# Optimization experiments

Measured on AMD Instinct MI355X. Metric: run time of the kernel, lower is better.

Reference implementation:

```python
import jax, jax.numpy as jnp
import numpy as np

D = 3            # sheaf stalk dimension
HIDDEN = 32      # hidden_channels
OUT_SHAPE = (3, 3)
N_ROWS = 300000  # N * d rows in x
E = 3000000      # edge_index entries (multiple of D)


def setup_inputs() -> dict:
    key = jax.random.key(0)
    k1, k2, k3 = jax.random.split(key, 3)
    x = jax.random.normal(k1, (N_ROWS, HIDDEN), dtype=jnp.float32)
    edge_index = jax.random.randint(k2, (2, E), 0, N_ROWS, dtype=jnp.int64)
    # linear1: nn.Linear(2*hidden, prod(out_shape), bias=False) -> weight [9, 64]
    W = jax.random.normal(k3, (int(np.prod(OUT_SHAPE)), 2 * HIDDEN), dtype=jnp.float32) * 0.1
    return {"x": x, "edge_index": edge_index, "W": W}


def reference(x, edge_index, W):
    src, dst = edge_index[0], edge_index[1]
    x_src = x[src]                       # [E, hidden] gather
    x_dst = x[dst]                       # [E, hidden] gather
    x_cat = jnp.concatenate([x_src, x_dst], axis=-1)         # [E, 2*hidden]
    x_cat = x_cat.reshape(-1, D, 2 * HIDDEN).sum(axis=1)      # [E/d, 2*hidden]
    maps = jnp.tanh(x_cat @ W.T)                              # [E/d, 9]
    return maps.reshape(-1, OUT_SHAPE[0], OUT_SHAPE[1])       # [E/d, 3, 3]
```

## Files before the change

kernel.cpp:

```cpp
#include <hip/hip_runtime.h>
#include <hip/hip_fp16.h>

#define HIDDEN 32
#define NOUT 9

__device__ __forceinline__ float fast_tanh(float v) {
    float e = __expf(2.0f * v);
    return 1.0f - __fdividef(2.0f, e + 1.0f);
}
__device__ __forceinline__ unsigned pack2f(float a, float b) {
    unsigned lo = __half_as_ushort(__float2half(a));
    unsigned hi = __half_as_ushort(__float2half(b));
    return lo | (hi << 16);
}
__device__ __forceinline__ float2 up2(unsigned u) {
    union { unsigned u; __half2 h; } cv; cv.u = u;
    return __half22float2(cv.h);
}

__device__ __forceinline__ unsigned q14(float y) {
    float t = fminf(fmaxf(y, -7.99f), 7.99f);
    return (unsigned)(__float2int_rn(t * 1024.f) + 8192);
}
__device__ __forceinline__ uint4 pack9(const float* y) {
    unsigned f0 = q14(y[0]), f1 = q14(y[1]), f2 = q14(y[2]);
    unsigned f3 = q14(y[3]), f4 = q14(y[4]), f5 = q14(y[5]);
    unsigned f6 = q14(y[6]), f7 = q14(y[7]), f8 = q14(y[8]);
    uint4 r;
    r.x = f0 | (f1 << 14) | (f2 << 28);
    r.y = (f2 >> 4) | (f3 << 10) | (f4 << 24);
    r.z = (f4 >> 8) | (f5 << 6) | (f6 << 20);
    r.w = (f6 >> 12) | (f7 << 2) | (f8 << 16);
    return r;
}
__device__ __forceinline__ unsigned ext14(const uint4& v, int j) {
    const int bit = 14 * j;
    if (bit + 14 <= 64) {
        unsigned long long u = ((unsigned long long)v.y << 32) | v.x;
        return (unsigned)(u >> bit) & 0x3FFFu;
    } else if (bit < 64) {
        unsigned long long u = ((unsigned long long)v.z << 32) | v.y;
        return (unsigned)(u >> (bit - 32)) & 0x3FFFu;
    } else {
        unsigned long long u = ((unsigned long long)v.w << 32) | v.z;
        return (unsigned)(u >> (bit - 64)) & 0x3FFFu;
    }
}

__global__ __launch_bounds__(256) void precompute_kernel(
    const float* __restrict__ x, const float* __restrict__ W,
    uint4* __restrict__ ys16, uint4* __restrict__ yd16, int NR)
{
    __shared__ float XL[256 * 33];
    __shared__ float Wl[NOUT * 64];
    for (int i = threadIdx.x; i < NOUT * 64; i += 256) Wl[i] = W[i];

    const int base = blockIdx.x * 256;
    const float4* Xv = reinterpret_cast<const float4*>(x);
    #pragma unroll
    for (int i = 0; i < 8; ++i) {
        int f = i * 256 + threadIdx.x;
        int row = f >> 3, ch = f & 7;
        float4 v = make_float4(0.f, 0.f, 0.f, 0.f);
        if (base + row < NR) v = Xv[(size_t)(base + row) * 8 + ch];
        float* p = &XL[row * 33 + ch * 4];
        p[0] = v.x; p[1] = v.y; p[2] = v.z; p[3] = v.w;
    }
    __syncthreads();

    const int row = base + threadIdx.x;
    if (row >= NR) return;

    float ys[NOUT], yd[NOUT];
    #pragma unroll
    for (int j = 0; j < NOUT; ++j) { ys[j] = 0.f; yd[j] = 0.f; }
    const float* xr = &XL[threadIdx.x * 33];
    #pragma unroll
    for (int c = 0; c < 32; ++c) {
        float xv = xr[c];
        #pragma unroll
        for (int j = 0; j < NOUT; ++j) {
            ys[j] += xv * Wl[j * 64 + c];
            yd[j] += xv * Wl[j * 64 + 32 + c];
        }
    }
    ys16[row] = pack9(ys);
    yd16[row] = pack9(yd);
}

__global__ __launch_bounds__(256) void passA_kernel(
    const uint4* __restrict__ ys16, const int* __restrict__ ei,
    unsigned* __restrict__ pw,
    unsigned short* __restrict__ ph,
    int G)
{
    int g = blockIdx.x * 256 + threadIdx.x;
    if (g >= G) return;
    const int* sp = ei + 3 * (size_t)g;
    int s0 = __builtin_nontemporal_load(sp);
    int s1 = __builtin_nontemporal_load(sp + 1);
    int s2 = __builtin_nontemporal_load(sp + 2);

    uint4 A0 = ys16[s0], A1 = ys16[s1], A2 = ys16[s2];

    float c[NOUT];
    #pragma unroll
    for (int j = 0; j < NOUT; ++j) {
        unsigned e = ext14(A0, j) + ext14(A1, j) + ext14(A2, j);
        c[j] = (float)(int)e * (1.f / 1024.f) - 24.f;
    }

    __builtin_nontemporal_store(pack2f(c[0], c[1]), pw + g);
    __builtin_nontemporal_store(pack2f(c[2], c[3]), pw + (size_t)G + g);
    __builtin_nontemporal_store(pack2f(c[4], c[5]), pw + 2 * (size_t)G + g);
    __builtin_nontemporal_store(pack2f(c[6], c[7]), pw + 3 * (size_t)G + g);
    __builtin_nontemporal_store(__half_as_ushort(__float2half(c[8])), ph + g);
}

__global__ __launch_bounds__(256) void passB_kernel(
    const uint4* __restrict__ yd16, const int* __restrict__ ei,
    const unsigned* __restrict__ pw, const unsigned short* __restrict__ ph,
    float* __restrict__ out, int G, int E)
{
    __shared__ float OL[256 * 9];
    const int t = threadIdx.x;
    const int g = blockIdx.x * 256 + t;

    if (g < G) {
        const int* dp = ei + (size_t)E + 3 * (size_t)g;
        int d0 = __builtin_nontemporal_load(dp);
        int d1 = __builtin_nontemporal_load(dp + 1);
        int d2 = __builtin_nontemporal_load(dp + 2);

        uint4 B0 = yd16[d0], B1 = yd16[d1], B2 = yd16[d2];

        unsigned pq0 = __builtin_nontemporal_load(pw + g);
        unsigned pq1 = __builtin_nontemporal_load(pw + (size_t)G + g);
        unsigned pq2 = __builtin_nontemporal_load(pw + 2 * (size_t)G + g);
        unsigned pq3 = __builtin_nontemporal_load(pw + 3 * (size_t)G + g);
        unsigned short pq4 = __builtin_nontemporal_load(ph + g);

        float c[NOUT];
        float2 tt;
        tt = up2(pq0); c[0] = tt.x; c[1] = tt.y;
        tt = up2(pq1); c[2] = tt.x; c[3] = tt.y;
        tt = up2(pq2); c[4] = tt.x; c[5] = tt.y;
        tt = up2(pq3); c[6] = tt.x; c[7] = tt.y;
        c[8] = __half2float(__ushort_as_half(pq4));

        #pragma unroll
        for (int j = 0; j < NOUT; ++j) {
            unsigned e = ext14(B0, j) + ext14(B1, j) + ext14(B2, j);
            c[j] += (float)(int)e * (1.f / 1024.f) - 24.f;
        }

        float* o = &OL[t * 9];
        #pragma unroll
        for (int j = 0; j < NOUT; ++j) o[j] = fast_tanh(c[j]);
    } else {
        float* o = &OL[t * 9];
        #pragma unroll
        for (int j = 0; j < NOUT; ++j) o[j] = 0.f;
    }
    __syncthreads();

    const size_t base = (size_t)blockIdx.x * 256 * 9;
    const size_t lim  = (size_t)G * 9;
    #pragma unroll
    for (int k = 0; k < 9; ++k) {
        size_t d = base + (size_t)k * 256 + t;
        if (d < lim)
            __builtin_nontemporal_store(OL[k * 256 + t], out + d);
    }
}

__global__ __launch_bounds__(256) void gather1_kernel(
    const uint4* __restrict__ ys16, const uint4* __restrict__ yd16,
    const int* __restrict__ ei, float* __restrict__ out, int G, int E)
{
    int g = blockIdx.x * 256 + threadIdx.x;
    if (g >= G) return;
    const int* sp = ei + 3 * (size_t)g;
    const int* dp = ei + (size_t)E + 3 * (size_t)g;
    int s0 = sp[0], s1 = sp[1], s2 = sp[2];
    int d0 = dp[0], d1 = dp[1], d2 = dp[2];
    uint4 A0 = ys16[s0], A1 = ys16[s1], A2 = ys16[s2];
    uint4 B0 = yd16[d0], B1 = yd16[d1], B2 = yd16[d2];
    float* o = out + (size_t)g * 9;
    #pragma unroll
    for (int j = 0; j < NOUT; ++j) {
        unsigned e = ext14(A0, j) + ext14(A1, j) + ext14(A2, j)
                   + ext14(B0, j) + ext14(B1, j) + ext14(B2, j);
        o[j] = fast_tanh((float)(int)e * (1.f / 1024.f) - 48.f);
    }
}

__device__ __forceinline__ float dot4(float4 a, float4 b) {
    return a.x * b.x + a.y * b.y + a.z * b.z + a.w * b.w;
}
__global__ __launch_bounds__(256) void sheaf_fallback(
    const float* __restrict__ x, const int* __restrict__ edge_index,
    const float* __restrict__ W, float* __restrict__ out, int G, int E)
{
    __shared__ float Wlds[NOUT * 64];
    for (int i = threadIdx.x; i < NOUT * 64; i += 256) Wlds[i] = W[i];
    __syncthreads();
    const int l = threadIdx.x & 7;
    const int s = (blockIdx.x * 256 + threadIdx.x) >> 3;
    const int g0 = 2 * s, g1 = 2 * s + 1;
    if (g0 >= G) return;
    const bool has1 = (g1 < G);
    const float4* Xv = reinterpret_cast<const float4*>(x);
    const float4* Wv = reinterpret_cast<const float4*>(Wlds);
    const int* sp = edge_index + 3 * g0;
    const int* dp = edge_index + E + 3 * g0;
    int s0 = sp[0], s1 = sp[1], s2 = sp[2], d0 = dp[0], d1 = dp[1], d2 = dp[2];
    int s3 = 0, s4 = 0, s5 = 0, d3 = 0, d4 = 0, d5 = 0;
    if (has1) { s3 = sp[3]; s4 = sp[4]; s5 = sp[5]; d3 = dp[3]; d4 = dp[4]; d5 = dp[5]; }
    float4 a0 = Xv[s0 * 8 + l], a1 = Xv[s1 * 8 + l], a2 = Xv[s2 * 8 + l];
    float4 b0 = Xv[d0 * 8 + l], b1 = Xv[d1 * 8 + l], b2 = Xv[d2 * 8 + l];
    float4 a3 = Xv[s3 * 8 + l], a4 = Xv[s4 * 8 + l], a5 = Xv[s5 * 8 + l];
    float4 b3 = Xv[d3 * 8 + l], b4 = Xv[d4 * 8 + l], b5 = Xv[d5 * 8 + l];
    float4 xs0, xd0, xs1, xd1;
    xs0.x = a0.x + a1.x + a2.x; xs0.y = a0.y + a1.y + a2.y;
    xs0.z = a0.z + a1.z + a2.z; xs0.w = a0.w + a1.w + a2.w;
    xd0.x = b0.x + b1.x + b2.x; xd0.y = b0.y + b1.y + b2.y;
    xd0.z = b0.z + b1.z + b2.z; xd0.w = b0.w + b1.w + b2.w;
    xs1.x = a3.x + a4.x + a5.x; xs1.y = a3.y + a4.y + a5.y;
    xs1.z = a3.z + a4.z + a5.z; xs1.w = a3.w + a4.w + a5.w;
    xd1.x = b3.x + b4.x + b5.x; xd1.y = b3.y + b4.y + b5.y;
    xd1.z = b3.z + b4.z + b5.z; xd1.w = b3.w + b4.w + b5.w;
    float my0 = 0.f, ex0 = 0.f, my1 = 0.f, ex1 = 0.f;
    #pragma unroll
    for (int j = 0; j < NOUT; ++j) {
        float4 ws = Wv[j * 16 + l];
        float4 wd = Wv[j * 16 + 8 + l];
        float t0 = dot4(xs0, ws) + dot4(xd0, wd);
        float t1 = dot4(xs1, ws) + dot4(xd1, wd);
        t0 += __shfl_xor(t0, 1); t1 += __shfl_xor(t1, 1);
        t0 += __shfl_xor(t0, 2); t1 += __shfl_xor(t1, 2);
        t0 += __shfl_xor(t0, 4); t1 += __shfl_xor(t1, 4);
        if (j < 8) { if (l == j) { my0 = t0; my1 = t1; } }
        else { ex0 = t0; ex1 = t1; }
    }
    out[g0 * 9 + l] = fast_tanh(my0);
    if (l == 0) out[g0 * 9 + 8] = fast_tanh(ex0);
    if (has1) {
        out[g1 * 9 + l] = fast_tanh(my1);
        if (l == 0) out[g1 * 9 + 8] = fast_tanh(ex1);
    }
}

extern "C" void kernel_launch(void* const* d_in, const int* in_sizes, int n_in,
                              void* d_out, int out_size, void* d_ws, size_t ws_size,
                              hipStream_t stream) {
    const float* x   = (const float*)d_in[0];
    const int*   ei  = (const int*)d_in[1];
    const float* W   = (const float*)d_in[2];
    float*       out = (float*)d_out;

    const int NR = in_sizes[0] / HIDDEN;
    const int E  = in_sizes[1] / 2;
    const int G  = E / 3;

    char* ws = (char*)d_ws;
    const size_t o_ys = 0;
    const size_t o_yd = o_ys + (size_t)NR * 16;
    const size_t o_pw = o_yd + (size_t)NR * 16;
    const size_t o_ph = o_pw + (size_t)G * 16;
    const size_t need_two = o_ph + (size_t)G * 2;
    const size_t need_one = o_pw;

    uint4*          ys16 = (uint4*)(ws + o_ys);
    uint4*          yd16 = (uint4*)(ws + o_yd);
    unsigned*       pw   = (unsigned*)(ws + o_pw);
    unsigned short* ph   = (unsigned short*)(ws + o_ph);

    const int gpre = (NR + 255) / 256;
    const int ggat = (G + 255) / 256;

    if (ws_size >= need_two) {
        hipLaunchKernelGGL(precompute_kernel, dim3(gpre), dim3(256), 0, stream,
                           x, W, ys16, yd16, NR);
        hipLaunchKernelGGL(passA_kernel, dim3(ggat), dim3(256), 0, stream,
                           ys16, ei, pw, ph, G);
        hipLaunchKernelGGL(passB_kernel, dim3(ggat), dim3(256), 0, stream,
                           yd16, ei, pw, ph, out, G, E);
    } else if (ws_size >= need_one) {
        hipLaunchKernelGGL(precompute_kernel, dim3(gpre), dim3(256), 0, stream,
                           x, W, ys16, yd16, NR);
        hipLaunchKernelGGL(gather1_kernel, dim3(ggat), dim3(256), 0, stream,
                           ys16, yd16, ei, out, G, E);
    } else {
        const int subwaves = (G + 1) / 2;
        const int blocks   = (subwaves + 31) / 32;
        hipLaunchKernelGGL(sheaf_fallback, dim3(blocks), dim3(256), 0, stream,
                           x, ei, W, out, G, E);
    }
}
```

Measured before the change: 77.65 us.

## Split precompute, overlap dst projection with src gather pass, pack partials

The fused precompute is split. A small kernel now computes only the source-side projection, and the destination-side projection runs as extra blocks inside the same launch as the source gather pass, so the two independent workloads share the GPU. The src partial sums are requantized to a 14-bit fixed-point format packed into one 16-byte record instead of five half-precision planes, and pass B reads that single vector. This aims to hide the dst projection behind the gather and reduce partial-sum traffic. It adds an extra re-read of x, and quantizing the intermediate sum to roughly 1/340 resolution costs some accuracy.

Result: slower. 102.6 us (+32.2%).

```diff
diff --git a/kernel.cpp b/kernel.cpp
--- a/kernel.cpp
+++ b/kernel.cpp
@@ -1,36 +1,22 @@
 #include <hip/hip_runtime.h>
-#include <hip/hip_fp16.h>
 
 #define HIDDEN 32
 #define NOUT 9
+
+typedef float    f4 __attribute__((ext_vector_type(4)));
+typedef unsigned u4 __attribute__((ext_vector_type(4)));
 
 __device__ __forceinline__ float fast_tanh(float v) {
     float e = __expf(2.0f * v);
     return 1.0f - __fdividef(2.0f, e + 1.0f);
 }
-__device__ __forceinline__ unsigned pack2f(float a, float b) {
-    unsigned lo = __half_as_ushort(__float2half(a));
-    unsigned hi = __half_as_ushort(__float2half(b));
-    return lo | (hi << 16);
-}
-__device__ __forceinline__ float2 up2(unsigned u) {
-    union { unsigned u; __half2 h; } cv; cv.u = u;
-    return __half22float2(cv.h);
-}
-
-__device__ __forceinline__ unsigned q14(float y) {
-    float t = fminf(fmaxf(y, -7.99f), 7.99f);
-    return (unsigned)(__float2int_rn(t * 1024.f) + 8192);
-}
-__device__ __forceinline__ uint4 pack9(const float* y) {
-    unsigned f0 = q14(y[0]), f1 = q14(y[1]), f2 = q14(y[2]);
-    unsigned f3 = q14(y[3]), f4 = q14(y[4]), f5 = q14(y[5]);
-    unsigned f6 = q14(y[6]), f7 = q14(y[7]), f8 = q14(y[8]);
+
+__device__ __forceinline__ uint4 pack9q(const unsigned* f) {
     uint4 r;
-    r.x = f0 | (f1 << 14) | (f2 << 28);
-    r.y = (f2 >> 4) | (f3 << 10) | (f4 << 24);
-    r.z = (f4 >> 8) | (f5 << 6) | (f6 << 20);
-    r.w = (f6 >> 12) | (f7 << 2) | (f8 << 16);
+    r.x = f[0] | (f[1] << 14) | (f[2] << 28);
+    r.y = (f[2] >> 4) | (f[3] << 10) | (f[4] << 24);
+    r.z = (f[4] >> 8) | (f[5] << 6) | (f[6] << 20);
+    r.w = (f[6] >> 12) | (f[7] << 2) | (f[8] << 16);
     return r;
 }
 __device__ __forceinline__ unsigned ext14(const uint4& v, int j) {
@@ -46,23 +32,30 @@
         return (unsigned)(u >> (bit - 64)) & 0x3FFFu;
     }
 }
-
-__global__ __launch_bounds__(256) void precompute_kernel(
+__device__ __forceinline__ unsigned q14(float y) {
+    float t = fminf(fmaxf(y, -7.99f), 7.99f);
+    return (unsigned)(__float2int_rn(t * 1024.f) + 8192);
+}
+
+__global__ __launch_bounds__(256) void preS_kernel(
     const float* __restrict__ x, const float* __restrict__ W,
-    uint4* __restrict__ ys16, uint4* __restrict__ yd16, int NR)
+    uint4* __restrict__ ys16, int NR)
 {
     __shared__ float XL[256 * 33];
-    __shared__ float Wl[NOUT * 64];
-    for (int i = threadIdx.x; i < NOUT * 64; i += 256) Wl[i] = W[i];
-
+    __shared__ float Wl[NOUT * 32];
+    for (int i = threadIdx.x; i < NOUT * 32; i += 256) {
+        int j = i >> 5, c = i & 31;
+        Wl[i] = W[j * 64 + c];
+    }
     const int base = blockIdx.x * 256;
-    const float4* Xv = reinterpret_cast<const float4*>(x);
+    const f4* Xv = (const f4*)x;
     #pragma unroll
     for (int i = 0; i < 8; ++i) {
-        int f = i * 256 + threadIdx.x;
-        int row = f >> 3, ch = f & 7;
-        float4 v = make_float4(0.f, 0.f, 0.f, 0.f);
-        if (base + row < NR) v = Xv[(size_t)(base + row) * 8 + ch];
+        int fi = i * 256 + threadIdx.x;
+        int row = fi >> 3, ch = fi & 7;
+        f4 v = {0.f, 0.f, 0.f, 0.f};
+        if (base + row < NR)
+            v = __builtin_nontemporal_load(Xv + (size_t)(base + row) * 8 + ch);
         float* p = &XL[row * 33 + ch * 4];
         p[0] = v.x; p[1] = v.y; p[2] = v.z; p[3] = v.w;
     }
@@ -70,57 +63,87 @@
 
     const int row = base + threadIdx.x;
     if (row >= NR) return;
-
-    float ys[NOUT], yd[NOUT];
-    #pragma unroll
-    for (int j = 0; j < NOUT; ++j) { ys[j] = 0.f; yd[j] = 0.f; }
+    float ys[NOUT];
+    #pragma unroll
+    for (int j = 0; j < NOUT; ++j) ys[j] = 0.f;
     const float* xr = &XL[threadIdx.x * 33];
     #pragma unroll
     for (int c = 0; c < 32; ++c) {
         float xv = xr[c];
         #pragma unroll
+        for (int j = 0; j < NOUT; ++j) ys[j] += xv * Wl[j * 32 + c];
+    }
+    unsigned f[NOUT];
+    #pragma unroll
+    for (int j = 0; j < NOUT; ++j) f[j] = q14(ys[j]);
+    ys16[row] = pack9q(f);
+}
+
+__global__ __launch_bounds__(256) void fused_kernel(
+    const float* __restrict__ x, const float* __restrict__ W,
+    const int* __restrict__ ei,
+    const uint4* __restrict__ ys16, uint4* __restrict__ yd16,
+    uint4* __restrict__ p16, int NR, int G, int PB)
+{
+    if ((int)blockIdx.x < PB) {
+        const int l  = threadIdx.x & 7;
+        const int sw = threadIdx.x >> 3;
+        const int base = blockIdx.x * 256;
+        const float4* Wv = reinterpret_cast<const float4*>(W);
+        float4 wd[NOUT];
+        #pragma unroll
+        for (int j = 0; j < NOUT; ++j) wd[j] = Wv[j * 16 + 8 + l];
+        const f4* Xv = (const f4*)x;
+        #pragma unroll
+        for (int r8 = 0; r8 < 8; ++r8) {
+            int row = base + 32 * r8 + sw;
+            if (row < NR) {
+                f4 v = __builtin_nontemporal_load(Xv + (size_t)row * 8 + l);
+                float yd[NOUT];
+                #pragma unroll
+                for (int j = 0; j < NOUT; ++j) {
+                    float t = v.x * wd[j].x + v.y * wd[j].y
+                            + v.z * wd[j].z + v.w * wd[j].w;
+                    t += __shfl_xor(t, 1);
+                    t += __shfl_xor(t, 2);
+                    t += __shfl_xor(t, 4);
+                    yd[j] = t;
+                }
+                if (l == 0) {
+                    unsigned f[NOUT];
+                    #pragma unroll
+                    for (int j = 0; j < NOUT; ++j) f[j] = q14(yd[j]);
+                    uint4 pk = pack9q(f);
+                    u4 pv = {pk.x, pk.y, pk.z, pk.w};
+                    __builtin_nontemporal_store(pv, (u4*)yd16 + row);
+                }
+            }
+        }
+    } else {
+        int g = ((int)blockIdx.x - PB) * 256 + threadIdx.x;
+        if (g >= G) return;
+        const int* sp = ei + 3 * (size_t)g;
+        int s0 = __builtin_nontemporal_load(sp);
+        int s1 = __builtin_nontemporal_load(sp + 1);
+        int s2 = __builtin_nontemporal_load(sp + 2);
+
+        uint4 A0 = ys16[s0], A1 = ys16[s1], A2 = ys16[s2];
+
+        unsigned f[NOUT];
+        #pragma unroll
         for (int j = 0; j < NOUT; ++j) {
-            ys[j] += xv * Wl[j * 64 + c];
-            yd[j] += xv * Wl[j * 64 + 32 + c];
+            unsigned e = ext14(A0, j) + ext14(A1, j) + ext14(A2, j);
+            f[j] = ((e * 340u + 512u) >> 10) + 32u;
         }
-    }
-    ys16[row] = pack9(ys);
-    yd16[row] = pack9(yd);
-}
-
-__global__ __launch_bounds__(256) void passA_kernel(
-    const uint4* __restrict__ ys16, const int* __restrict__ ei,
-    unsigned* __restrict__ pw,
-    unsigned short* __restrict__ ph,
-    int G)
-{
-    int g = blockIdx.x * 256 + threadIdx.x;
-    if (g >= G) return;
-    const int* sp = ei + 3 * (size_t)g;
-    int s0 = __builtin_nontemporal_load(sp);
-    int s1 = __builtin_nontemporal_load(sp + 1);
-    int s2 = __builtin_nontemporal_load(sp + 2);
-
-    uint4 A0 = ys16[s0], A1 = ys16[s1], A2 = ys16[s2];
-
-    float c[NOUT];
-    #pragma unroll
-    for (int j = 0; j < NOUT; ++j) {
-        unsigned e = ext14(A0, j) + ext14(A1, j) + ext14(A2, j);
-        c[j] = (float)(int)e * (1.f / 1024.f) - 24.f;
-    }
-
-    __builtin_nontemporal_store(pack2f(c[0], c[1]), pw + g);
-    __builtin_nontemporal_store(pack2f(c[2], c[3]), pw + (size_t)G + g);
-    __builtin_nontemporal_store(pack2f(c[4], c[5]), pw + 2 * (size_t)G + g);
-    __builtin_nontemporal_store(pack2f(c[6], c[7]), pw + 3 * (size_t)G + g);
-    __builtin_nontemporal_store(__half_as_ushort(__float2half(c[8])), ph + g);
+        uint4 pk = pack9q(f);
+        u4 pv = {pk.x, pk.y, pk.z, pk.w};
+        __builtin_nontemporal_store(pv, (u4*)p16 + g);
+    }
 }
 
 __global__ __launch_bounds__(256) void passB_kernel(
     const uint4* __restrict__ yd16, const int* __restrict__ ei,
-    const unsigned* __restrict__ pw, const unsigned short* __restrict__ ph,
-    float* __restrict__ out, int G, int E)
+    const uint4* __restrict__ p16, float* __restrict__ out, int G, int E)
 {
     __shared__ float OL[256 * 9];
     const int t = threadIdx.x;
@@ -133,30 +156,17 @@
         int d2 = __builtin_nontemporal_load(dp + 2);
 
         uint4 B0 = yd16[d0], B1 = yd16[d1], B2 = yd16[d2];
-
-        unsigned pq0 = __builtin_nontemporal_load(pw + g);
-        unsigned pq1 = __builtin_nontemporal_load(pw + (size_t)G + g);
-        unsigned pq2 = __builtin_nontemporal_load(pw + 2 * (size_t)G + g);
-        unsigned pq3 = __builtin_nontemporal_load(pw + 3 * (size_t)G + g);
-        unsigned short pq4 = __builtin_nontemporal_load(ph + g);
-
-        float c[NOUT];
-        float2 tt;
-        tt = up2(pq0); c[0] = tt.x; c[1] = tt.y;
-        tt = up2(pq1); c[2] = tt.x; c[3] = tt.y;
-        tt = up2(pq2); c[4] = tt.x; c[5] = tt.y;
-        tt = up2(pq3); c[6] = tt.x; c[7] = tt.y;
-        c[8] = __half2float(__ushort_as_half(pq4));
-
+        u4 P = __builtin_nontemporal_load((const u4*)p16 + g);
+        uint4 Pq; Pq.x = P.x; Pq.y = P.y; Pq.z = P.z; Pq.w = P.w;
+
+        float* o = &OL[t * 9];
         #pragma unroll
         for (int j = 0; j < NOUT; ++j) {
             unsigned e = ext14(B0, j) + ext14(B1, j) + ext14(B2, j);
-            c[j] += (float)(int)e * (1.f / 1024.f) - 24.f;
+            float cdst = (float)(int)e * (1.f / 1024.f) - 24.f;
+            float csrc = (float)((int)ext14(Pq, j) - 8192) * (1.f / 340.f);
+            o[j] = fast_tanh(csrc + cdst);
         }
-
-        float* o = &OL[t * 9];
-        #pragma unroll
-        for (int j = 0; j < NOUT; ++j) o[j] = fast_tanh(c[j]);
     } else {
         float* o = &OL[t * 9];
         #pragma unroll
@@ -266,30 +276,30 @@
     char* ws = (char*)d_ws;
     const size_t o_ys = 0;
     const size_t o_yd = o_ys + (size_t)NR * 16;
-    const size_t o_pw = o_yd + (size_t)NR * 16;
-    const size_t o_ph = o_pw + (size_t)G * 16;
-    const size_t need_two = o_ph + (size_t)G * 2;
-    const size_t need_one = o_pw;
-
-    uint4*          ys16 = (uint4*)(ws + o_ys);
-    uint4*          yd16 = (uint4*)(ws + o_yd);
-    unsigned*       pw   = (unsigned*)(ws + o_pw);
-    unsigned short* ph   = (unsigned short*)(ws + o_ph);
-
-    const int gpre = (NR + 255) / 256;
-    const int ggat = (G + 255) / 256;
+    const size_t o_p  = o_yd + (size_t)NR * 16;
+    const size_t need_two = o_p + (size_t)G * 16;
+    const size_t need_one = o_p;
+
+    uint4* ys16 = (uint4*)(ws + o_ys);
+    uint4* yd16 = (uint4*)(ws + o_yd);
+    uint4* p16  = (uint4*)(ws + o_p);
+
+    const int PB = (NR + 255) / 256;
+    const int GB = (G + 255) / 256;
 
     if (ws_size >= need_two) {
-        hipLaunchKernelGGL(precompute_kernel, dim3(gpre), dim3(256), 0, stream,
-                           x, W, ys16, yd16, NR);
-        hipLaunchKernelGGL(passA_kernel, dim3(ggat), dim3(256), 0, stream,
-                           ys16, ei, pw, ph, G);
-        hipLaunchKernelGGL(passB_kernel, dim3(ggat), dim3(256), 0, stream,
-                           yd16, ei, pw, ph, out, G, E);
+        hipLaunchKernelGGL(preS_kernel, dim3(PB), dim3(256), 0, stream,
+                           x, W, ys16, NR);
+        hipLaunchKernelGGL(fused_kernel, dim3(PB + GB), dim3(256), 0, stream,
+                           x, W, ei, ys16, yd16, p16, NR, G, PB);
+        hipLaunchKernelGGL(passB_kernel, dim3(GB), dim3(256), 0, stream,
+                           yd16, ei, p16, out, G, E);
     } else if (ws_size >= need_one) {
-        hipLaunchKernelGGL(precompute_kernel, dim3(gpre), dim3(256), 0, stream,
-                           x, W, ys16, yd16, NR);
-        hipLaunchKernelGGL(gather1_kernel, dim3(ggat), dim3(256), 0, stream,
+        hipLaunchKernelGGL(preS_kernel, dim3(PB), dim3(256), 0, stream,
+                           x, W, ys16, NR);
+        hipLaunchKernelGGL(fused_kernel, dim3(PB), dim3(256), 0, stream,
+                           x, W, ei, ys16, yd16, p16, NR, 0, PB);
+        hipLaunchKernelGGL(gather1_kernel, dim3(GB), dim3(256), 0, stream,
                            ys16, yd16, ei, out, G, E);
     } else {
         const int subwaves = (G + 1) / 2;
```

## Fuse source and destination gather passes into one kernel with LDS-staged output

Applied to the files above, without the earlier changes.

Replaces the two-pass scheme, where pass A gathered source projections into an fp16 intermediate and pass B read it back, with a single gather kernel. That kernel loads both src and dst packed 14-bit projections, sums them, applies tanh, and stages the output through LDS for coalesced nontemporal stores. This removes the intermediate write and read traffic and one kernel launch, at the cost of each thread issuing six random gathers instead of three, which lowers the memory-level locality the split pass gave to each table. The x loads in precompute also become nontemporal.

Measured after the change: 98.11 us. +26.3%, slower.

```diff
diff --git a/kernel.cpp b/kernel.cpp
--- a/kernel.cpp
+++ b/kernel.cpp
@@ -1,36 +1,21 @@
 #include <hip/hip_runtime.h>
-#include <hip/hip_fp16.h>
 
 #define HIDDEN 32
 #define NOUT 9
+
+typedef float f4 __attribute__((ext_vector_type(4)));
 
 __device__ __forceinline__ float fast_tanh(float v) {
     float e = __expf(2.0f * v);
     return 1.0f - __fdividef(2.0f, e + 1.0f);
 }
-__device__ __forceinline__ unsigned pack2f(float a, float b) {
-    unsigned lo = __half_as_ushort(__float2half(a));
-    unsigned hi = __half_as_ushort(__float2half(b));
-    return lo | (hi << 16);
-}
-__device__ __forceinline__ float2 up2(unsigned u) {
-    union { unsigned u; __half2 h; } cv; cv.u = u;
-    return __half22float2(cv.h);
-}
-
-__device__ __forceinline__ unsigned q14(float y) {
-    float t = fminf(fmaxf(y, -7.99f), 7.99f);
-    return (unsigned)(__float2int_rn(t * 1024.f) + 8192);
-}
-__device__ __forceinline__ uint4 pack9(const float* y) {
-    unsigned f0 = q14(y[0]), f1 = q14(y[1]), f2 = q14(y[2]);
-    unsigned f3 = q14(y[3]), f4 = q14(y[4]), f5 = q14(y[5]);
-    unsigned f6 = q14(y[6]), f7 = q14(y[7]), f8 = q14(y[8]);
+
+__device__ __forceinline__ uint4 pack9q(const unsigned* f) {
     uint4 r;
-    r.x = f0 | (f1 << 14) | (f2 << 28);
-    r.y = (f2 >> 4) | (f3 << 10) | (f4 << 24);
-    r.z = (f4 >> 8) | (f5 << 6) | (f6 << 20);
-    r.w = (f6 >> 12) | (f7 << 2) | (f8 << 16);
+    r.x = f[0] | (f[1] << 14) | (f[2] << 28);
+    r.y = (f[2] >> 4) | (f[3] << 10) | (f[4] << 24);
+    r.z = (f[4] >> 8) | (f[5] << 6) | (f[6] << 20);
+    r.w = (f[6] >> 12) | (f[7] << 2) | (f[8] << 16);
     return r;
 }
 __device__ __forceinline__ unsigned ext14(const uint4& v, int j) {
@@ -46,6 +31,10 @@
         return (unsigned)(u >> (bit - 64)) & 0x3FFFu;
     }
 }
+__device__ __forceinline__ unsigned q14(float y) {
+    float t = fminf(fmaxf(y, -7.99f), 7.99f);
+    return (unsigned)(__float2int_rn(t * 1024.f) + 8192);
+}
 
 __global__ __launch_bounds__(256) void precompute_kernel(
     const float* __restrict__ x, const float* __restrict__ W,
@@ -56,13 +45,14 @@
     for (int i = threadIdx.x; i < NOUT * 64; i += 256) Wl[i] = W[i];
 
     const int base = blockIdx.x * 256;
-    const float4* Xv = reinterpret_cast<const float4*>(x);
+    const f4* Xv = (const f4*)x;
     #pragma unroll
     for (int i = 0; i < 8; ++i) {
-        int f = i * 256 + threadIdx.x;
-        int row = f >> 3, ch = f & 7;
-        float4 v = make_float4(0.f, 0.f, 0.f, 0.f);
-        if (base + row < NR) v = Xv[(size_t)(base + row) * 8 + ch];
+        int fi = i * 256 + threadIdx.x;
+        int row = fi >> 3, ch = fi & 7;
+        f4 v = {0.f, 0.f, 0.f, 0.f};
+        if (base + row < NR)
+            v = __builtin_nontemporal_load(Xv + (size_t)(base + row) * 8 + ch);
         float* p = &XL[row * 33 + ch * 4];
         p[0] = v.x; p[1] = v.y; p[2] = v.z; p[3] = v.w;
     }
@@ -84,79 +74,41 @@
             yd[j] += xv * Wl[j * 64 + 32 + c];
         }
     }
-    ys16[row] = pack9(ys);
-    yd16[row] = pack9(yd);
-}
-
-__global__ __launch_bounds__(256) void passA_kernel(
-    const uint4* __restrict__ ys16, const int* __restrict__ ei,
-    unsigned* __restrict__ pw,
-    unsigned short* __restrict__ ph,
-    int G)
-{
-    int g = blockIdx.x * 256 + threadIdx.x;
-    if (g >= G) return;
-    const int* sp = ei + 3 * (size_t)g;
-    int s0 = __builtin_nontemporal_load(sp);
-    int s1 = __builtin_nontemporal_load(sp + 1);
-    int s2 = __builtin_nontemporal_load(sp + 2);
-
-    uint4 A0 = ys16[s0], A1 = ys16[s1], A2 = ys16[s2];
-
-    float c[NOUT];
-    #pragma unroll
-    for (int j = 0; j < NOUT; ++j) {
-        unsigned e = ext14(A0, j) + ext14(A1, j) + ext14(A2, j);
-        c[j] = (float)(int)e * (1.f / 1024.f) - 24.f;
-    }
-
-    __builtin_nontemporal_store(pack2f(c[0], c[1]), pw + g);
-    __builtin_nontemporal_store(pack2f(c[2], c[3]), pw + (size_t)G + g);
-    __builtin_nontemporal_store(pack2f(c[4], c[5]), pw + 2 * (size_t)G + g);
-    __builtin_nontemporal_store(pack2f(c[6], c[7]), pw + 3 * (size_t)G + g);
-    __builtin_nontemporal_store(__half_as_ushort(__float2half(c[8])), ph + g);
-}
-
-__global__ __launch_bounds__(256) void passB_kernel(
-    const uint4* __restrict__ yd16, const int* __restrict__ ei,
-    const unsigned* __restrict__ pw, const unsigned short* __restrict__ ph,
-    float* __restrict__ out, int G, int E)
+    unsigned fs[NOUT], fd[NOUT];
+    #pragma unroll
+    for (int j = 0; j < NOUT; ++j) { fs[j] = q14(ys[j]); fd[j] = q14(yd[j]); }
+    ys16[row] = pack9q(fs);
+    yd16[row] = pack9q(fd);
+}
+
+__global__ __launch_bounds__(256) void gather1_kernel(
+    const uint4* __restrict__ ys16, const uint4* __restrict__ yd16,
+    const int* __restrict__ ei, float* __restrict__ out, int G, int E)
 {
     __shared__ float OL[256 * 9];
     const int t = threadIdx.x;
     const int g = blockIdx.x * 256 + t;
 
     if (g < G) {
+        const int* sp = ei + 3 * (size_t)g;
         const int* dp = ei + (size_t)E + 3 * (size_t)g;
+        int s0 = __builtin_nontemporal_load(sp);
+        int s1 = __builtin_nontemporal_load(sp + 1);
+        int s2 = __builtin_nontemporal_load(sp + 2);
         int d0 = __builtin_nontemporal_load(dp);
         int d1 = __builtin_nontemporal_load(dp + 1);
         int d2 = __builtin_nontemporal_load(dp + 2);
 
+        uint4 A0 = ys16[s0], A1 = ys16[s1], A2 = ys16[s2];
         uint4 B0 = yd16[d0], B1 = yd16[d1], B2 = yd16[d2];
 
-        unsigned pq0 = __builtin_nontemporal_load(pw + g);
-        unsigned pq1 = __builtin_nontemporal_load(pw + (size_t)G + g);
-        unsigned pq2 = __builtin_nontemporal_load(pw + 2 * (size_t)G + g);
-        unsigned pq3 = __builtin_nontemporal_load(pw + 3 * (size_t)G + g);
-        unsigned short pq4 = __builtin_nontemporal_load(ph + g);
-
-        float c[NOUT];
-        float2 tt;
-        tt = up2(pq0); c[0] = tt.x; c[1] = tt.y;
-        tt = up2(pq1); c[2] = tt.x; c[3] = tt.y;
-        tt = up2(pq2); c[4] = tt.x; c[5] = tt.y;
-        tt = up2(pq3); c[6] = tt.x; c[7] = tt.y;
-        c[8] = __half2float(__ushort_as_half(pq4));
-
+        float* o = &OL[t * 9];
         #pragma unroll
         for (int j = 0; j < NOUT; ++j) {
-            unsigned e = ext14(B0, j) + ext14(B1, j) + ext14(B2, j);
-            c[j] += (float)(int)e * (1.f / 1024.f) - 24.f;
+            unsigned e = ext14(A0, j) + ext14(A1, j) + ext14(A2, j)
+                       + ext14(B0, j) + ext14(B1, j) + ext14(B2, j);
+            o[j] = fast_tanh((float)(int)e * (1.f / 1024.f) - 48.f);
         }
-
-        float* o = &OL[t * 9];
-        #pragma unroll
-        for (int j = 0; j < NOUT; ++j) o[j] = fast_tanh(c[j]);
     } else {
         float* o = &OL[t * 9];
         #pragma unroll
@@ -171,27 +123,6 @@
         size_t d = base + (size_t)k * 256 + t;
         if (d < lim)
             __builtin_nontemporal_store(OL[k * 256 + t], out + d);
-    }
-}
-
-__global__ __launch_bounds__(256) void gather1_kernel(
-    const uint4* __restrict__ ys16, const uint4* __restrict__ yd16,
-    const int* __restrict__ ei, float* __restrict__ out, int G, int E)
-{
-    int g = blockIdx.x * 256 + threadIdx.x;
-    if (g >= G) return;
-    const int* sp = ei + 3 * (size_t)g;
-    const int* dp = ei + (size_t)E + 3 * (size_t)g;
-    int s0 = sp[0], s1 = sp[1], s2 = sp[2];
-    int d0 = dp[0], d1 = dp[1], d2 = dp[2];
-    uint4 A0 = ys16[s0], A1 = ys16[s1], A2 = ys16[s2];
-    uint4 B0 = yd16[d0], B1 = yd16[d1], B2 = yd16[d2];
-    float* o = out + (size_t)g * 9;
-    #pragma unroll
-    for (int j = 0; j < NOUT; ++j) {
-        unsigned e = ext14(A0, j) + ext14(A1, j) + ext14(A2, j)
-                   + ext14(B0, j) + ext14(B1, j) + ext14(B2, j);
-        o[j] = fast_tanh((float)(int)e * (1.f / 1024.f) - 48.f);
     }
 }
 
@@ -266,30 +197,18 @@
     char* ws = (char*)d_ws;
     const size_t o_ys = 0;
     const size_t o_yd = o_ys + (size_t)NR * 16;
-    const size_t o_pw = o_yd + (size_t)NR * 16;
-    const size_t o_ph = o_pw + (size_t)G * 16;
-    const size_t need_two = o_ph + (size_t)G * 2;
-    const size_t need_one = o_pw;
-
-    uint4*          ys16 = (uint4*)(ws + o_ys);
-    uint4*          yd16 = (uint4*)(ws + o_yd);
-    unsigned*       pw   = (unsigned*)(ws + o_pw);
-    unsigned short* ph   = (unsigned short*)(ws + o_ph);
-
-    const int gpre = (NR + 255) / 256;
-    const int ggat = (G + 255) / 256;
-
-    if (ws_size >= need_two) {
-        hipLaunchKernelGGL(precompute_kernel, dim3(gpre), dim3(256), 0, stream,
+    const size_t need = o_yd + (size_t)NR * 16;
+
+    uint4* ys16 = (uint4*)(ws + o_ys);
+    uint4* yd16 = (uint4*)(ws + o_yd);
+
+    const int PB = (NR + 255) / 256;
+    const int GB = (G + 255) / 256;
+
+    if (ws_size >= need) {
+        hipLaunchKernelGGL(precompute_kernel, dim3(PB), dim3(256), 0, stream,
                            x, W, ys16, yd16, NR);
-        hipLaunchKernelGGL(passA_kernel, dim3(ggat), dim3(256), 0, stream,
-                           ys16, ei, pw, ph, G);
-        hipLaunchKernelGGL(passB_kernel, dim3(ggat), dim3(256), 0, stream,
-                           yd16, ei, pw, ph, out, G, E);
-    } else if (ws_size >= need_one) {
-        hipLaunchKernelGGL(precompute_kernel, dim3(gpre), dim3(256), 0, stream,
-                           x, W, ys16, yd16, NR);
-        hipLaunchKernelGGL(gather1_kernel, dim3(ggat), dim3(256), 0, stream,
+        hipLaunchKernelGGL(gather1_kernel, dim3(GB), dim3(256), 0, stream,
                            ys16, yd16, ei, out, G, E);
     } else {
         const int subwaves = (G + 1) / 2;
```
